# Kernel optimization log

Hardware: AMD Instinct MI355X
Metric: run time of the kernel (lower is better)

Reference implementation:

```python
import jax, jax.numpy as jnp
import numpy as np

EMB = 256
IN_CH = 256
CTX_D = 128


def setup_inputs() -> dict:
    key = jax.random.key(0)
    ks = jax.random.split(key, 12)
    b, c, h, w = 16, IN_CH, 48, 48
    seq = 2048
    s = 0.02
    return {
        "x": jax.random.normal(ks[0], (b, c, h, w), jnp.float32),
        "context": jax.random.normal(ks[1], (b, seq, CTX_D), jnp.float32),
        "pad_mask": jax.random.bernoulli(ks[2], 0.1, (b, h * w, seq)),
        "W_in": jax.random.normal(ks[3], (EMB, IN_CH), jnp.float32) * s,   # 1x1 conv weight
        "b_in": jnp.zeros((EMB,), jnp.float32),
        "Wq": jax.random.normal(ks[4], (EMB, EMB), jnp.float32) * s,
        "bq": jnp.zeros((EMB,), jnp.float32),
        "Wk": jax.random.normal(ks[5], (EMB, CTX_D), jnp.float32) * s,
        "bk": jnp.zeros((EMB,), jnp.float32),
        "Wv": jax.random.normal(ks[6], (EMB, CTX_D), jnp.float32) * s,
        "bv": jnp.zeros((EMB,), jnp.float32),
        "W_out": jax.random.normal(ks[7], (IN_CH, EMB), jnp.float32) * s,  # 1x1 conv weight
        "b_out": jnp.zeros((IN_CH,), jnp.float32),
    }


def reference(x, context, pad_mask, W_in, b_in, Wq, bq, Wk, bk, Wv, bv, W_out, b_out):
    b, c, h, w = x.shape
    scale = EMB ** (-0.5)
    # proj_in: 1x1 conv == channel matmul; then b c h w -> b (h w) c
    xt = jnp.einsum('bchw,ec->behw', x, W_in) + b_in[None, :, None, None]
    xt = xt.reshape(b, EMB, h * w).transpose(0, 2, 1)          # [b, hw, emb]
    Q = xt @ Wq.T + bq                                          # [b, hw, emb]
    K = context @ Wk.T + bk                                     # [b, seq, emb]
    V = context @ Wv.T + bv                                     # [b, seq, emb]
    att = jnp.einsum('bid,bjd->bij', Q, K) * scale              # [b, hw, seq]
    att = jnp.where(pad_mask, jnp.float32(-1e9), att)
    att = jax.nn.softmax(att, axis=-1)
    out = jnp.einsum('bij,bjd->bid', att, V)                    # [b, hw, emb]
    out = out.transpose(0, 2, 1).reshape(b, EMB, h, w)
    out = jnp.einsum('behw,ce->bchw', out, W_out) + b_out[None, :, None, None]
    return out, att
```

## Files before the change

### kernel.cpp

```cpp
#include <hip/hip_runtime.h>

typedef unsigned short u16;
typedef unsigned int   u32;
typedef __attribute__((ext_vector_type(8))) __bf16 bf16x8;
typedef __attribute__((ext_vector_type(4))) float  f32x4;

#define BB   16
#define CH   256
#define HW   2304
#define SEQ  2048
#define EMB  256
#define CTXD 128
#define OUT0 9437184

#define MFMA(a,b,c) __builtin_amdgcn_mfma_f32_16x16x32_bf16(a,b,c,0,0,0)

__device__ __forceinline__ u16 f2bf(float f){
  u32 u = __builtin_bit_cast(u32, f);
  u += 0x7fffu + ((u >> 16) & 1u);
  return (u16)(u >> 16);
}
__device__ __forceinline__ float bf2f(u32 us){ return __builtin_bit_cast(float, us << 16); }

__device__ __forceinline__ bf16x8 ld16(const u16* p){
  uint4 q = *reinterpret_cast<const uint4*>(p);
  return __builtin_bit_cast(bf16x8, q);
}
__device__ __forceinline__ bf16x8 ld16c(const char* p){
  uint4 q = *reinterpret_cast<const uint4*>(p);
  return __builtin_bit_cast(bf16x8, q);
}
__device__ __forceinline__ bf16x8 mk8(float a0,float a1,float a2,float a3,
                                      float a4,float a5,float a6,float a7){
  uint4 q;
  q.x = (u32)f2bf(a0) | ((u32)f2bf(a1) << 16);
  q.y = (u32)f2bf(a2) | ((u32)f2bf(a3) << 16);
  q.z = (u32)f2bf(a4) | ((u32)f2bf(a5) << 16);
  q.w = (u32)f2bf(a6) | ((u32)f2bf(a7) << 16);
  return __builtin_bit_cast(bf16x8, q);
}
__device__ __forceinline__ void gload16(const u16* g, u16* l){
  __builtin_amdgcn_global_load_lds(
      (const __attribute__((address_space(1))) unsigned int*)(const void*)g,
      (__attribute__((address_space(3))) unsigned int*)(void*)l, 16, 0, 0);
}

__global__ __launch_bounds__(256) void k_prep(
    const float* __restrict__ Wq, const float* __restrict__ W_in,
    const float* __restrict__ b_in, const float* __restrict__ bq,
    const float* __restrict__ Wk, const float* __restrict__ Wv,
    const float* __restrict__ Wout,
    u16* __restrict__ WqinBf, u16* __restrict__ WkBf, u16* __restrict__ WvBf,
    u16* __restrict__ WoutBf, float* __restrict__ bq_eff)
{
  int blk = blockIdx.x, t = threadIdx.x;
  const float SC = 0.0625f;
  if (blk < 256) {
    int e = blk, c = t;
    float s = 0.f;
    #pragma unroll 8
    for (int f = 0; f < 256; f++) s += Wq[e*256+f] * W_in[f*256+c];
    WqinBf[e*256+c] = f2bf(s * SC);
    __shared__ float rb[4];
    float pb = Wq[e*256+t] * b_in[t];
    pb += __shfl_xor(pb, 1);  pb += __shfl_xor(pb, 2);
    pb += __shfl_xor(pb, 4);  pb += __shfl_xor(pb, 8);
    pb += __shfl_xor(pb, 16); pb += __shfl_xor(pb, 32);
    if ((t & 63) == 0) rb[t >> 6] = pb;
    __syncthreads();
    if (t == 0) bq_eff[e] = (rb[0]+rb[1]+rb[2]+rb[3] + bq[e]) * SC;
  } else {
    u32 flat = (u32)(blk - 256) * 256 + t;
    for (u32 idx = flat; idx < 131072u; idx += 16384u) {
      if (idx < 32768u)       WkBf[idx]          = f2bf(Wk[idx]);
      else if (idx < 65536u)  WvBf[idx - 32768u] = f2bf(Wv[idx - 32768u]);
      else                    WoutBf[idx - 65536u] = f2bf(Wout[idx - 65536u]);
    }
  }
}

__global__ __launch_bounds__(256) void k_qproj(
    const float* __restrict__ x, const u16* __restrict__ WqinBf,
    const float* __restrict__ bq_eff, u16* __restrict__ Qbf)
{
  int b = blockIdx.y, ibase = blockIdx.x * 64;
  int t = threadIdx.x, wv = t >> 6, lane = t & 63, g4 = lane >> 4, r16 = lane & 15;
  int e0 = wv * 64;
  f32x4 acc[4][4] = {};
  #pragma unroll 2
  for (int kk = 0; kk < 8; kk++) {
    bf16x8 a[4];
    #pragma unroll
    for (int m = 0; m < 4; m++)
      a[m] = ld16(WqinBf + (size_t)(e0 + m*16 + r16) * 256 + kk*32 + g4*8);
    bf16x8 bb[4];
    #pragma unroll
    for (int n = 0; n < 4; n++) {
      const float* xp = x + ((size_t)b*CH + kk*32 + g4*8) * HW + ibase + n*16 + r16;
      bb[n] = mk8(xp[0], xp[HW], xp[2*HW], xp[3*HW], xp[4*HW], xp[5*HW], xp[6*HW], xp[7*HW]);
    }
    #pragma unroll
    for (int m = 0; m < 4; m++)
      #pragma unroll
      for (int n = 0; n < 4; n++)
        acc[m][n] = MFMA(a[m], bb[n], acc[m][n]);
  }
  #pragma unroll
  for (int m = 0; m < 4; m++) {
    int e = e0 + m*16 + g4*4;
    float b0 = bq_eff[e], b1 = bq_eff[e+1], b2 = bq_eff[e+2], b3 = bq_eff[e+3];
    #pragma unroll
    for (int n = 0; n < 4; n++) {
      int i = ibase + n*16 + r16;
      u32 lo = (u32)f2bf(acc[m][n][0] + b0) | ((u32)f2bf(acc[m][n][1] + b1) << 16);
      u32 hi = (u32)f2bf(acc[m][n][2] + b2) | ((u32)f2bf(acc[m][n][3] + b3) << 16);
      *(uint2*)(Qbf + ((size_t)b*HW + i) * EMB + e) = make_uint2(lo, hi);
    }
  }
}

__global__ __launch_bounds__(512) void k_kvproj(
    const float* __restrict__ ctx, const u16* __restrict__ WkBf, const u16* __restrict__ WvBf,
    const float* __restrict__ bk, const float* __restrict__ bv,
    u16* __restrict__ Kbf, u16* __restrict__ Vtb)
{
  int b = blockIdx.y, sbase = blockIdx.x * 64;
  int t = threadIdx.x, wv = t >> 6, lane = t & 63, g4 = lane >> 4, r16 = lane & 15;
  bool isV = wv >= 4;
  int e0 = (wv & 3) * 64;
  const u16* Wsel = isV ? WvBf : WkBf;
  f32x4 acc[4][4] = {};
  #pragma unroll
  for (int kk = 0; kk < 4; kk++) {
    bf16x8 a[4];
    #pragma unroll
    for (int m = 0; m < 4; m++)
      a[m] = ld16(Wsel + (size_t)(e0 + m*16 + r16) * 128 + kk*32 + g4*8);
    bf16x8 bb[4];
    #pragma unroll
    for (int n = 0; n < 4; n++) {
      const float* cp = ctx + ((size_t)b*SEQ + sbase + n*16 + r16) * CTXD + kk*32 + g4*8;
      float4 lo = *(const float4*)cp;
      float4 hi = *(const float4*)(cp + 4);
      bb[n] = mk8(lo.x, lo.y, lo.z, lo.w, hi.x, hi.y, hi.z, hi.w);
    }
    #pragma unroll
    for (int m = 0; m < 4; m++)
      #pragma unroll
      for (int n = 0; n < 4; n++)
        acc[m][n] = MFMA(a[m], bb[n], acc[m][n]);
  }
  if (!isV) {
    #pragma unroll
    for (int m = 0; m < 4; m++) {
      int e = e0 + m*16 + g4*4;
      float b0 = bk[e], b1 = bk[e+1], b2 = bk[e+2], b3 = bk[e+3];
      #pragma unroll
      for (int n = 0; n < 4; n++) {
        int s = sbase + n*16 + r16;
        u32 lo = (u32)f2bf(acc[m][n][0] + b0) | ((u32)f2bf(acc[m][n][1] + b1) << 16);
        u32 hi = (u32)f2bf(acc[m][n][2] + b2) | ((u32)f2bf(acc[m][n][3] + b3) << 16);
        *(uint2*)(Kbf + ((size_t)b*SEQ + s) * EMB + e) = make_uint2(lo, hi);
      }
    }
  } else {
    #pragma unroll
    for (int m = 0; m < 4; m++) {
      #pragma unroll
      for (int r = 0; r < 4; r++) {
        int e = e0 + m*16 + g4*4 + r;
        float bvv = bv[e];
        #pragma unroll
        for (int n = 0; n < 4; n++) {
          int s = sbase + n*16 + r16;
          Vtb[((size_t)b*EMB + e) * SEQ + s] = f2bf(acc[m][n][r] + bvv);
        }
      }
    }
  }
}

__global__ __launch_bounds__(512, 4) void k_qk(
    const u16* __restrict__ Qbf, const u16* __restrict__ Kbf,
    const int* __restrict__ mask, float* __restrict__ dout,
    float* __restrict__ gpart)
{
  __shared__ u16 lsA[128*64];
  __shared__ u16 lsB[128*64];
  __shared__ float red[4][128];

  int bid = blockIdx.x;
  int work = (bid & 7) * 576 + (bid >> 3);
  int b = work / 288, rem = work % 288;
  int mt = rem / 16, jt = rem % 16;
  int mbase = mt * 128, jbase = jt * 128;
  size_t bH = (size_t)b * HW, bS = (size_t)b * SEQ;

  int t = threadIdx.x, lane = t & 63, wv = t >> 6, g4 = lane >> 4, r16 = lane & 15;
  int wr = wv >> 2, wc = wv & 3;

  int mreg[4][2][4];
  {
    const int* mp = mask + (bH + mbase + wr*64 + g4*4) * SEQ + jbase + wc*32 + r16;
    #pragma unroll
    for (int m = 0; m < 4; m++)
      #pragma unroll
      for (int n = 0; n < 2; n++)
        #pragma unroll
        for (int r = 0; r < 4; r++)
          mreg[m][n][r] = mp[(size_t)(m*16 + r) * SEQ + n*16];
  }

  int i0 = t, i1 = t + 512;
  int r0 = i0 >> 3, c0 = (i0 & 7) ^ (r0 & 7);
  int r1 = i1 >> 3, c1 = (i1 & 7) ^ (r1 & 7);
  const u16* qs0 = Qbf + (bH + mbase + r0) * 256 + c0*8;
  const u16* qs1 = Qbf + (bH + mbase + r1) * 256 + c1*8;
  const u16* ks0 = Kbf + (bS + jbase + r0) * 256 + c0*8;
  const u16* ks1 = Kbf + (bS + jbase + r1) * 256 + c1*8;
  u16 *dA0 = lsA + i0*8, *dA1 = lsA + i1*8, *dB0 = lsB + i0*8, *dB1 = lsB + i1*8;

  const char* lA = (const char*)lsA;
  const char* lB = (const char*)lsB;

  f32x4 acc[4][2] = {};
  #pragma unroll 1
  for (int ks = 0; ks < 4; ks++) {
    gload16(qs0 + ks*64, dA0);
    gload16(qs1 + ks*64, dA1);
    gload16(ks0 + ks*64, dB0);
    gload16(ks1 + ks*64, dB1);
    __syncthreads();
    #pragma unroll
    for (int kk = 0; kk < 2; kk++) {
      bf16x8 af[4], bf[2];
      #pragma unroll
      for (int m = 0; m < 4; m++) {
        int row = wr*64 + m*16 + r16;
        af[m] = ld16c(lA + row*128 + (((kk<<2)|g4) ^ (row&7))*16);
      }
      #pragma unroll
      for (int n = 0; n < 2; n++) {
        int row = wc*32 + n*16 + r16;
        bf[n] = ld16c(lB + row*128 + (((kk<<2)|g4) ^ (row&7))*16);
      }
      #pragma unroll
      for (int m = 0; m < 4; m++)
        #pragma unroll
        for (int n = 0; n < 2; n++)
          acc[m][n] = MFMA(af[m], bf[n], acc[m][n]);
    }
    __syncthreads();
  }

  u16* Ebase = (u16*)(dout + OUT0);
  float part[4][4] = {};
  #pragma unroll
  for (int m = 0; m < 4; m++)
    #pragma unroll
    for (int n = 0; n < 2; n++)
      #pragma unroll
      for (int r = 0; r < 4; r++) {
        float e = mreg[m][n][r] ? 0.f : __expf(acc[m][n][r]);
        part[m][r] += e;
        int i = wr*64 + m*16 + g4*4 + r;
        int j = jbase + wc*32 + n*16 + r16;
        Ebase[(bH + mbase + i) * 4096 + 2048 + j] = f2bf(e);
      }
  #pragma unroll
  for (int m = 0; m < 4; m++)
    #pragma unroll
    for (int r = 0; r < 4; r++) {
      float v = part[m][r];
      v += __shfl_xor(v, 1); v += __shfl_xor(v, 2);
      v += __shfl_xor(v, 4); v += __shfl_xor(v, 8);
      if (r16 == 0) red[wc][wr*64 + m*16 + g4*4 + r] = v;
    }
  __syncthreads();
  if (t < 128) {
    float tot = red[0][t] + red[1][t] + red[2][t] + red[3][t];
    gpart[(bH + mbase + t) * 16 + jt] = tot;
  }
}

__global__ __launch_bounds__(512, 6) void k_pv(
    const u16* __restrict__ Vtb, const float* __restrict__ gpart,
    float* __restrict__ dout, u16* __restrict__ Obf)
{
  __shared__ u16 lsE[2][64*64];
  __shared__ float invl[64];

  int bid = blockIdx.x;
  int work = (bid & 7) * 72 + (bid >> 3);
  int b = work / 36, mt = work % 36;
  int mbase = mt * 64;
  size_t bH = (size_t)b * HW;

  int t = threadIdx.x, lane = t & 63, wv = t >> 6, g4 = lane >> 4, r16 = lane & 15;
  int wm = wv >> 2, we = wv & 3;

  if (t < 64) {
    const float4* pp = (const float4*)(gpart + (bH + mbase + t) * 16);
    float4 p0 = pp[0], p1 = pp[1], p2 = pp[2], p3 = pp[3];
    invl[t] = 1.f / (p0.x+p0.y+p0.z+p0.w + p1.x+p1.y+p1.z+p1.w
                   + p2.x+p2.y+p2.z+p2.w + p3.x+p3.y+p3.z+p3.w);
  }

  const u16* Ebase = (const u16*)(dout + OUT0);
  float* attb = dout + OUT0;
  int rE = t >> 3, cE = (t & 7) ^ (rE & 7);
  const u16* esrc = Ebase + (bH + mbase + rE) * 4096 + 2048 + cE*8;
  const u16* Vb = Vtb + (size_t)b * EMB * SEQ;
  int srow = t >> 3;
  u32 sxor = (u32)((t & 7) ^ (srow & 7)) * 16;
  float* arow = attb + (bH + mbase + srow) * 2048 + (t & 7) * 8;

  gload16(esrc, lsE[0] + t*8);
  __syncthreads();

  f32x4 acc[2][4] = {};
  int cur = 0;
  #pragma unroll 1
  for (int c = 0; c < 32; c++) {
    int kb = c * 64;
    if (c < 31) gload16(esrc + kb + 64, lsE[cur ^ 1] + t*8);
    const char* lE = (const char*)lsE[cur];
    #pragma unroll
    for (int kk = 0; kk < 2; kk++) {
      bf16x8 aE[2];
      #pragma unroll
      for (int m = 0; m < 2; m++) {
        int row = wm*32 + m*16 + r16;
        aE[m] = ld16c(lE + row*128 + (((kk<<2)|g4) ^ (row&7))*16);
      }
      #pragma unroll
      for (int n = 0; n < 4; n++) {
        bf16x8 bV = ld16(Vb + (size_t)(we*64 + n*16 + r16) * SEQ + kb + kk*32 + g4*8);
        acc[0][n] = MFMA(aE[0], bV, acc[0][n]);
        acc[1][n] = MFMA(aE[1], bV, acc[1][n]);
      }
    }
    {
      float iv = invl[srow];
      const u16* ep = (const u16*)(lE + srow*128 + sxor);
      float4 o0, o1;
      o0.x = bf2f(ep[0]) * iv; o0.y = bf2f(ep[1]) * iv;
      o0.z = bf2f(ep[2]) * iv; o0.w = bf2f(ep[3]) * iv;
      o1.x = bf2f(ep[4]) * iv; o1.y = bf2f(ep[5]) * iv;
      o1.z = bf2f(ep[6]) * iv; o1.w = bf2f(ep[7]) * iv;
      *(float4*)(arow + kb) = o0;
      *(float4*)(arow + kb + 4) = o1;
    }
    __syncthreads();
    cur ^= 1;
  }

  #pragma unroll
  for (int m = 0; m < 2; m++)
    #pragma unroll
    for (int n = 0; n < 4; n++)
      #pragma unroll
      for (int r = 0; r < 4; r++) {
        int i = wm*32 + m*16 + g4*4 + r;
        int e = we*64 + n*16 + r16;
        Obf[(bH + mbase + i) * 256 + e] = f2bf(acc[m][n][r] * invl[i]);
      }
}

__global__ __launch_bounds__(256) void k_outproj(
    const u16* __restrict__ Obf, const u16* __restrict__ WoutBf,
    const float* __restrict__ bout, float* __restrict__ out)
{
  int b = blockIdx.y, ibase = blockIdx.x * 64;
  int t = threadIdx.x, wv = t >> 6, lane = t & 63, g4 = lane >> 4, r16 = lane & 15;
  int c0 = wv * 64;
  f32x4 acc[4][4] = {};
  #pragma unroll 2
  for (int kk = 0; kk < 8; kk++) {
    bf16x8 a[4];
    #pragma unroll
    for (int m = 0; m < 4; m++)
      a[m] = ld16(WoutBf + (size_t)(c0 + m*16 + r16) * 256 + kk*32 + g4*8);
    bf16x8 bb[4];
    #pragma unroll
    for (int n = 0; n < 4; n++)
      bb[n] = ld16(Obf + ((size_t)b*HW + ibase + n*16 + r16) * EMB + kk*32 + g4*8);
    #pragma unroll
    for (int m = 0; m < 4; m++)
      #pragma unroll
      for (int n = 0; n < 4; n++)
        acc[m][n] = MFMA(a[m], bb[n], acc[m][n]);
  }
  #pragma unroll
  for (int m = 0; m < 4; m++) {
    #pragma unroll
    for (int r = 0; r < 4; r++) {
      int c = c0 + m*16 + g4*4 + r;
      float bo = bout[c];
      #pragma unroll
      for (int n = 0; n < 4; n++) {
        int i = ibase + n*16 + r16;
        out[((size_t)b*CH + c) * HW + i] = acc[m][n][r] + bo;
      }
    }
  }
}

extern "C" void kernel_launch(void* const* d_in, const int* in_sizes, int n_in,
                              void* d_out, int out_size, void* d_ws, size_t ws_size,
                              hipStream_t stream)
{
  const float* x    = (const float*)d_in[0];
  const float* ctx  = (const float*)d_in[1];
  const int*   mask = (const int*)  d_in[2];
  const float* W_in = (const float*)d_in[3];
  const float* b_in = (const float*)d_in[4];
  const float* Wq   = (const float*)d_in[5];
  const float* bq   = (const float*)d_in[6];
  const float* Wk   = (const float*)d_in[7];
  const float* bk   = (const float*)d_in[8];
  const float* Wv   = (const float*)d_in[9];
  const float* bv   = (const float*)d_in[10];
  const float* Wout = (const float*)d_in[11];
  const float* bout = (const float*)d_in[12];
  float* out = (float*)d_out;

  char* ws = (char*)d_ws;
  size_t off = 0;
  auto alloc = [&](size_t bytes) -> void* {
    void* p = ws + off;
    off += (bytes + 255) & ~(size_t)255;
    return p;
  };
  u16*   WqinBf = (u16*)  alloc(256*256*2);
  u16*   WkBf   = (u16*)  alloc(256*128*2);
  u16*   WvBf   = (u16*)  alloc(256*128*2);
  u16*   WoutBf = (u16*)  alloc(256*256*2);
  float* bq_eff = (float*)alloc(256*4);
  float* gpart  = (float*)alloc((size_t)BB*HW*16*4);
  u16*   Qbf    = (u16*)  alloc((size_t)BB*HW*EMB*2);
  u16*   Kbf    = (u16*)  alloc((size_t)BB*SEQ*EMB*2);
  u16*   Vtb    = (u16*)  alloc((size_t)BB*EMB*SEQ*2);
  if (off > ws_size) return;

  k_prep<<<dim3(320), dim3(256), 0, stream>>>(Wq, W_in, b_in, bq, Wk, Wv, Wout,
                                              WqinBf, WkBf, WvBf, WoutBf, bq_eff);
  k_qproj<<<dim3(36, 16), dim3(256), 0, stream>>>(x, WqinBf, bq_eff, Qbf);
  k_kvproj<<<dim3(32, 16), dim3(512), 0, stream>>>(ctx, WkBf, WvBf, bk, bv, Kbf, Vtb);
  k_qk<<<dim3(4608), dim3(512), 0, stream>>>(Qbf, Kbf, mask, out, gpart);
  k_pv<<<dim3(576), dim3(512), 0, stream>>>(Vtb, gpart, out, Qbf );
  k_outproj<<<dim3(36, 16), dim3(256), 0, stream>>>(Qbf , WoutBf, bout, out);
}
```

Baseline: 502.2 us.

## Split PV into inverse-sum, LDS-tiled 128x128 PV GEMM, and separate attention normalize pass

The fused PV kernel becomes three kernels. The first computes per-row inverse softmax sums. The second is a 128x128-tiled bf16 GEMM that stages both the exponentials E and V in LDS, replacing the per-wave global loads of V. The third rewrites the fp32 normalized attention rows in place from the bf16 E stored in the upper half of each row. This aims to raise MFMA reuse and cut V traffic, at the cost of reading E a second time and launching two extra kernels.

```diff
diff --git a/kernel.cpp b/kernel.cpp
--- a/kernel.cpp
+++ b/kernel.cpp
@@ -283,88 +283,120 @@
   }
 }
 
-__global__ __launch_bounds__(512, 6) void k_pv(
-    const u16* __restrict__ Vtb, const float* __restrict__ gpart,
-    float* __restrict__ dout, u16* __restrict__ Obf)
-{
-  __shared__ u16 lsE[2][64*64];
-  __shared__ float invl[64];
+__global__ __launch_bounds__(256) void k_inv(
+    const float* __restrict__ gpart, float* __restrict__ invrs)
+{
+  int row = blockIdx.x * 256 + threadIdx.x;
+  const float4* pp = (const float4*)(gpart + (size_t)row * 16);
+  float4 p0 = pp[0], p1 = pp[1], p2 = pp[2], p3 = pp[3];
+  invrs[row] = 1.f / (p0.x+p0.y+p0.z+p0.w + p1.x+p1.y+p1.z+p1.w
+                    + p2.x+p2.y+p2.z+p2.w + p3.x+p3.y+p3.z+p3.w);
+}
+
+__global__ __launch_bounds__(256, 3) void k_pv(
+    const u16* __restrict__ Vtb, const float* __restrict__ invrs,
+    const float* __restrict__ dout, u16* __restrict__ Obf)
+{
+  __shared__ u16 lsA[128*64];
+  __shared__ u16 lsB[128*64];
 
   int bid = blockIdx.x;
   int work = (bid & 7) * 72 + (bid >> 3);
-  int b = work / 36, mt = work % 36;
-  int mbase = mt * 64;
+  int b = work / 36, rem = work % 36;
+  int mt = rem >> 1, nt = rem & 1;
+  int mbase = mt * 128, ebase = nt * 128;
   size_t bH = (size_t)b * HW;
 
   int t = threadIdx.x, lane = t & 63, wv = t >> 6, g4 = lane >> 4, r16 = lane & 15;
-  int wm = wv >> 2, we = wv & 3;
-
-  if (t < 64) {
-    const float4* pp = (const float4*)(gpart + (bH + mbase + t) * 16);
-    float4 p0 = pp[0], p1 = pp[1], p2 = pp[2], p3 = pp[3];
-    invl[t] = 1.f / (p0.x+p0.y+p0.z+p0.w + p1.x+p1.y+p1.z+p1.w
-                   + p2.x+p2.y+p2.z+p2.w + p3.x+p3.y+p3.z+p3.w);
-  }
+  int wr = wv >> 1, wc = wv & 1;
 
   const u16* Ebase = (const u16*)(dout + OUT0);
-  float* attb = dout + OUT0;
-  int rE = t >> 3, cE = (t & 7) ^ (rE & 7);
-  const u16* esrc = Ebase + (bH + mbase + rE) * 4096 + 2048 + cE*8;
-  const u16* Vb = Vtb + (size_t)b * EMB * SEQ;
-  int srow = t >> 3;
-  u32 sxor = (u32)((t & 7) ^ (srow & 7)) * 16;
-  float* arow = attb + (bH + mbase + srow) * 2048 + (t & 7) * 8;
-
-  gload16(esrc, lsE[0] + t*8);
-  __syncthreads();
-
-  f32x4 acc[2][4] = {};
-  int cur = 0;
+  int rs[4], cs[4];
+  #pragma unroll
+  for (int q = 0; q < 4; q++) {
+    int idx = q*256 + t;
+    rs[q] = idx >> 3;
+    cs[q] = (idx & 7) ^ (rs[q] & 7);
+  }
+  const char* lA = (const char*)lsA;
+  const char* lB = (const char*)lsB;
+
+  f32x4 acc[4][4] = {};
   #pragma unroll 1
-  for (int c = 0; c < 32; c++) {
-    int kb = c * 64;
-    if (c < 31) gload16(esrc + kb + 64, lsE[cur ^ 1] + t*8);
-    const char* lE = (const char*)lsE[cur];
+  for (int ks = 0; ks < 32; ks++) {
+    int kb = ks * 64;
+    #pragma unroll
+    for (int q = 0; q < 4; q++) {
+      gload16(Ebase + (bH + mbase + rs[q]) * 4096 + 2048 + kb + cs[q]*8,
+              lsA + (q*256 + t)*8);
+      gload16(Vtb + ((size_t)b*EMB + ebase + rs[q]) * SEQ + kb + cs[q]*8,
+              lsB + (q*256 + t)*8);
+    }
+    __syncthreads();
     #pragma unroll
     for (int kk = 0; kk < 2; kk++) {
-      bf16x8 aE[2];
-      #pragma unroll
-      for (int m = 0; m < 2; m++) {
-        int row = wm*32 + m*16 + r16;
-        aE[m] = ld16c(lE + row*128 + (((kk<<2)|g4) ^ (row&7))*16);
+      bf16x8 af[4], bf[4];
+      #pragma unroll
+      for (int m = 0; m < 4; m++) {
+        int row = wr*64 + m*16 + r16;
+        af[m] = ld16c(lA + row*128 + (((kk<<2)|g4) ^ (row&7))*16);
       }
       #pragma unroll
       for (int n = 0; n < 4; n++) {
-        bf16x8 bV = ld16(Vb + (size_t)(we*64 + n*16 + r16) * SEQ + kb + kk*32 + g4*8);
-        acc[0][n] = MFMA(aE[0], bV, acc[0][n]);
-        acc[1][n] = MFMA(aE[1], bV, acc[1][n]);
-      }
-    }
-    {
-      float iv = invl[srow];
-      const u16* ep = (const u16*)(lE + srow*128 + sxor);
-      float4 o0, o1;
-      o0.x = bf2f(ep[0]) * iv; o0.y = bf2f(ep[1]) * iv;
-      o0.z = bf2f(ep[2]) * iv; o0.w = bf2f(ep[3]) * iv;
-      o1.x = bf2f(ep[4]) * iv; o1.y = bf2f(ep[5]) * iv;
-      o1.z = bf2f(ep[6]) * iv; o1.w = bf2f(ep[7]) * iv;
-      *(float4*)(arow + kb) = o0;
-      *(float4*)(arow + kb + 4) = o1;
+        int row = wc*64 + n*16 + r16;
+        bf[n] = ld16c(lB + row*128 + (((kk<<2)|g4) ^ (row&7))*16);
+      }
+      #pragma unroll
+      for (int m = 0; m < 4; m++)
+        #pragma unroll
+        for (int n = 0; n < 4; n++)
+          acc[m][n] = MFMA(af[m], bf[n], acc[m][n]);
     }
     __syncthreads();
-    cur ^= 1;
-  }
-
-  #pragma unroll
-  for (int m = 0; m < 2; m++)
-    #pragma unroll
-    for (int n = 0; n < 4; n++)
-      #pragma unroll
-      for (int r = 0; r < 4; r++) {
-        int i = wm*32 + m*16 + g4*4 + r;
-        int e = we*64 + n*16 + r16;
-        Obf[(bH + mbase + i) * 256 + e] = f2bf(acc[m][n][r] * invl[i]);
-      }
+  }
+
+  #pragma unroll
+  for (int m = 0; m < 4; m++)
+    #pragma unroll
+    for (int r = 0; r < 4; r++) {
+      int i = wr*64 + m*16 + g4*4 + r;
+      float iv = invrs[bH + mbase + i];
+      #pragma unroll
+      for (int n = 0; n < 4; n++) {
+        int e = ebase + wc*64 + n*16 + r16;
+        Obf[(bH + mbase + i) * 256 + e] = f2bf(acc[m][n][r] * iv);
+      }
+    }
+}
+
+__global__ __launch_bounds__(512, 4) void k_att(
+    const float* __restrict__ invrs, float* __restrict__ dout)
+{
+  int bid = blockIdx.x;
+  int work = (bid & 7) * 288 + (bid >> 3);
+  int t = threadIdx.x, wv = t >> 6, lane = t & 63;
+
+  #pragma unroll
+  for (int rr = 0; rr < 2; rr++) {
+    size_t row = (size_t)work * 16 + wv * 2 + rr;
+    const u16* Erow = (const u16*)(dout + OUT0) + row * 4096 + 2048;
+    float* arow = dout + OUT0 + row * 2048;
+    float iv = invrs[row];
+    uint2 raw[8];
+    #pragma unroll
+    for (int seg = 0; seg < 8; seg++)
+      raw[seg] = *(const uint2*)(Erow + (size_t)(seg*64 + lane) * 4);
+    asm volatile("s_waitcnt vmcnt(0)" ::: "memory");
+    #pragma unroll
+    for (int seg = 0; seg < 8; seg++) {
+      float4 o;
+      o.x = bf2f(raw[seg].x & 0xffffu) * iv;
+      o.y = bf2f(raw[seg].x >> 16)     * iv;
+      o.z = bf2f(raw[seg].y & 0xffffu) * iv;
+      o.w = bf2f(raw[seg].y >> 16)     * iv;
+      *(float4*)(arow + (size_t)(seg*64 + lane) * 4) = o;
+    }
+  }
 }
 
 __global__ __launch_bounds__(256) void k_outproj(
@@ -438,6 +470,7 @@
   u16*   WoutBf = (u16*)  alloc(256*256*2);
   float* bq_eff = (float*)alloc(256*4);
   float* gpart  = (float*)alloc((size_t)BB*HW*16*4);
+  float* invrs  = (float*)alloc((size_t)BB*HW*4);
   u16*   Qbf    = (u16*)  alloc((size_t)BB*HW*EMB*2);
   u16*   Kbf    = (u16*)  alloc((size_t)BB*SEQ*EMB*2);
   u16*   Vtb    = (u16*)  alloc((size_t)BB*EMB*SEQ*2);
@@ -448,6 +481,8 @@
   k_qproj<<<dim3(36, 16), dim3(256), 0, stream>>>(x, WqinBf, bq_eff, Qbf);
   k_kvproj<<<dim3(32, 16), dim3(512), 0, stream>>>(ctx, WkBf, WvBf, bk, bv, Kbf, Vtb);
   k_qk<<<dim3(4608), dim3(512), 0, stream>>>(Qbf, Kbf, mask, out, gpart);
-  k_pv<<<dim3(576), dim3(512), 0, stream>>>(Vtb, gpart, out, Qbf );
+  k_inv<<<dim3(144), dim3(256), 0, stream>>>(gpart, invrs);
+  k_pv<<<dim3(576), dim3(256), 0, stream>>>(Vtb, invrs, out, Qbf );
+  k_att<<<dim3(2304), dim3(512), 0, stream>>>(invrs, out);
   k_outproj<<<dim3(36, 16), dim3(256), 0, stream>>>(Qbf , WoutBf, bout, out);
 }
```

After: 410.6 us. 18.2% less time.
